# Performance work log

Measured on AMD Instinct MI355X. Metric: run time of the kernel, lower is better.

Reference implementation:

```python
import jax, jax.numpy as jnp
import numpy as np

ITER_NUM = 512
BATCH = 65536
HIDDEN = 256
DELTA_T = 0.1


def setup_inputs() -> dict:
    key = jax.random.key(0)
    k1, k2, k3, k4 = jax.random.split(key, 4)
    inflows = jax.random.uniform(k1, (ITER_NUM, BATCH, 1), dtype=jnp.float32)
    storage0 = jax.random.uniform(k2, (BATCH,), dtype=jnp.float32)
    W1 = jax.random.normal(k3, (2, HIDDEN), dtype=jnp.float32) * 0.5
    b1 = jnp.zeros((HIDDEN,), dtype=jnp.float32)
    W2 = jax.random.normal(k4, (HIDDEN, 1), dtype=jnp.float32) * 0.1
    b2 = jnp.zeros((1,), dtype=jnp.float32)
    return {"inflows": inflows, "storage0": storage0, "W1": W1, "b1": b1, "W2": W2, "b2": b2}


def reference(inflows, storage0, W1, b1, W2, b2):
    # AnnModel: Linear(nx,hidden) -> ReLU -> Linear(hidden,ny)
    def mlp(x):  # x: (B, 2)
        h = jax.nn.relu(x @ W1 + b1)          # (B, H)
        return h @ W2 + b2                     # (B, 1)

    def step(storage, inflow):  # storage: (B,1), inflow: (B,1)
        x = jnp.concatenate([inflow, storage], axis=1)      # (B, 2)
        outflow = mlp(x)                                     # (B, 1)
        storage_new = DELTA_T * (inflow - outflow) + storage # water balance update
        return storage_new, (storage_new, outflow)

    s0 = storage0[:, None]  # (B, 1)
    _, (stor_seq, outflows) = jax.lax.scan(step, s0, inflows)
    storages = jnp.concatenate([s0[None], stor_seq], axis=0)  # (T+1, B, 1)
    return storages, outflows
```

## Files before the change

### kernel.cpp

```cpp
#include <hip/hip_runtime.h>

#define DT 0.1f

typedef float v2f __attribute__((ext_vector_type(2)));

__global__ void pack_weights(const float* __restrict__ W1, const float* __restrict__ b1,
                             const float* __restrict__ W2, float4* __restrict__ ws, int hidden) {
    int j = blockIdx.x * blockDim.x + threadIdx.x;
    if (j < hidden) {
        ws[j] = make_float4(W1[j], W1[hidden + j], b1[j], W2[j]);
    }
}

template <int CTRL>
__device__ __forceinline__ float dpp_add(float x) {
    int v = __builtin_amdgcn_mov_dpp(__float_as_int(x), CTRL, 0xf, 0xf, true);
    return x + __int_as_float(v);
}

__global__ __launch_bounds__(256) void waterbalance(
    const float* __restrict__ inflows, const float* __restrict__ storage0,
    const float4* __restrict__ ws, const float* __restrict__ b2,
    float* __restrict__ out_storages, float* __restrict__ out_outflows,
    int iters, int batch)
{
    const int tid = blockIdx.x * blockDim.x + threadIdx.x;
    const int e = tid >> 3;
    const int p = tid & 7;
    if (e >= batch) return;

    v2f wx[16], wy[16], wb[16], w2[16];
    #pragma unroll
    for (int r = 0; r < 16; ++r) {
        float4 a = ws[p * 32 + 2 * r];
        float4 b = ws[p * 32 + 2 * r + 1];
        wx[r] = (v2f){a.x, b.x};
        wy[r] = (v2f){a.y, b.y};
        wb[r] = (v2f){a.z, b.z};
        w2[r] = (v2f){a.w, b.w};
    }
    const float b2v = b2[0];

    float s = storage0[e];
    if (p == 0) out_storages[e] = s;

    float inflow = inflows[e];
    for (int t = 0; t < iters; ++t) {
        float next = (t + 1 < iters) ? inflows[(size_t)(t + 1) * batch + e] : 0.0f;

        const v2f in2 = (v2f){inflow, inflow};
        const v2f s2  = (v2f){s, s};
        v2f acc0 = (v2f)(0.0f);
        v2f acc1 = (v2f)(0.0f);
        const v2f zero2 = (v2f)(0.0f);

        #pragma unroll
        for (int r = 0; r < 16; r += 2) {
            v2f z0 = __builtin_elementwise_fma(in2, wx[r],
                        __builtin_elementwise_fma(s2, wy[r], wb[r]));
            z0 = __builtin_elementwise_max(z0, zero2);
            acc0 = __builtin_elementwise_fma(z0, w2[r], acc0);

            v2f z1 = __builtin_elementwise_fma(in2, wx[r + 1],
                        __builtin_elementwise_fma(s2, wy[r + 1], wb[r + 1]));
            z1 = __builtin_elementwise_max(z1, zero2);
            acc1 = __builtin_elementwise_fma(z1, w2[r + 1], acc1);
        }

        float part = (acc0.x + acc0.y) + (acc1.x + acc1.y);
        part = dpp_add<0xB1>(part);
        part = dpp_add<0x4E>(part);
        part = dpp_add<0x141>(part);
        const float outflow = part + b2v;

        s = fmaf(DT, inflow - outflow, s);

        if (p == 0) {
            out_outflows[(size_t)t * batch + e] = outflow;
            out_storages[(size_t)(t + 1) * batch + e] = s;
        }
        inflow = next;
    }
}

extern "C" void kernel_launch(void* const* d_in, const int* in_sizes, int n_in,
                              void* d_out, int out_size, void* d_ws, size_t ws_size,
                              hipStream_t stream) {
    const float* inflows  = (const float*)d_in[0];
    const float* storage0 = (const float*)d_in[1];
    const float* W1       = (const float*)d_in[2];
    const float* b1       = (const float*)d_in[3];
    const float* W2       = (const float*)d_in[4];
    const float* b2       = (const float*)d_in[5];

    int batch  = in_sizes[1];
    int iters  = in_sizes[0] / batch;
    int hidden = in_sizes[3];

    float4* ws = (float4*)d_ws;
    pack_weights<<<(hidden + 255) / 256, 256, 0, stream>>>(W1, b1, W2, ws, hidden);

    float* out_storages = (float*)d_out;
    float* out_outflows = out_storages + (size_t)(iters + 1) * batch;

    int threads = batch * 8;
    waterbalance<<<(threads + 255) / 256, 256, 0, stream>>>(
        inflows, storage0, ws, b2, out_storages, out_outflows, iters, batch);
}
```

Before: 1.059 ms.

## Prefetch inflows in chunks of eight and force packed FMA via inline asm

Restructures the time loop into chunks of 8 steps. The next chunk's 8 inflow values are loaded ahead while the current chunk computes, which hides global-load latency behind the serial recurrence better than a one-step prefetch. The MLP FMAs are forced to v_pk_fma_f32 through inline asm, and empty asm barriers pin the weights in VGPRs. The outputs use incremented pointers, which removes index arithmetic. This costs more registers and loses some compiler scheduling freedom around the asm blocks.

```diff
diff --git a/kernel.cpp b/kernel.cpp
--- a/kernel.cpp
+++ b/kernel.cpp
@@ -10,6 +10,12 @@
     if (j < hidden) {
         ws[j] = make_float4(W1[j], W1[hidden + j], b1[j], W2[j]);
     }
+}
+
+__device__ __forceinline__ v2f pk_fma(v2f a, v2f b, v2f c) {
+    v2f d;
+    asm("v_pk_fma_f32 %0, %1, %2, %3" : "=v"(d) : "v"(a), "v"(b), "v"(c));
+    return d;
 }
 
 template <int CTRL>
@@ -39,47 +45,105 @@
         wb[r] = (v2f){a.z, b.z};
         w2[r] = (v2f){a.w, b.w};
     }
+    #pragma unroll
+    for (int r = 0; r < 16; ++r) {
+        asm("" : "+v"(wx[r]), "+v"(wy[r]), "+v"(wb[r]), "+v"(w2[r]));
+    }
+
     const float b2v = b2[0];
 
     float s = storage0[e];
     if (p == 0) out_storages[e] = s;
 
-    float inflow = inflows[e];
-    for (int t = 0; t < iters; ++t) {
-        float next = (t + 1 < iters) ? inflows[(size_t)(t + 1) * batch + e] : 0.0f;
+    const float* __restrict__ inp = inflows + e;
+    float* __restrict__ po = out_outflows + e;
+    float* __restrict__ ps = out_storages + (size_t)batch + e;
 
+    const int nchunk = iters >> 3;
+    const int tail_start = nchunk << 3;
+
+    float buf[8];
+    #pragma unroll
+    for (int r = 0; r < 8; ++r) buf[r] = inp[(size_t)r * batch];
+
+    for (int c = 0; c < nchunk; ++c) {
+        float nb[8];
+        if (c + 1 < nchunk) {
+            const float* q = inp + (size_t)(c + 1) * 8 * batch;
+            #pragma unroll
+            for (int r = 0; r < 8; ++r) nb[r] = q[(size_t)r * batch];
+        } else {
+            #pragma unroll
+            for (int r = 0; r < 8; ++r) nb[r] = 0.0f;
+        }
+
+        #pragma unroll
+        for (int r = 0; r < 8; ++r) {
+            const float inflow = buf[r];
+            const v2f in2 = (v2f){inflow, inflow};
+            const v2f s2  = (v2f){s, s};
+            const v2f zero2 = (v2f)(0.0f);
+            v2f acc0 = (v2f)(0.0f);
+            v2f acc1 = (v2f)(0.0f);
+
+            #pragma unroll
+            for (int g = 0; g < 16; g += 2) {
+                v2f z0 = pk_fma(in2, wx[g], pk_fma(s2, wy[g], wb[g]));
+                z0 = __builtin_elementwise_max(z0, zero2);
+                acc0 = pk_fma(z0, w2[g], acc0);
+
+                v2f z1 = pk_fma(in2, wx[g + 1], pk_fma(s2, wy[g + 1], wb[g + 1]));
+                z1 = __builtin_elementwise_max(z1, zero2);
+                acc1 = pk_fma(z1, w2[g + 1], acc1);
+            }
+
+            float part = (acc0.x + acc1.x) + (acc0.y + acc1.y);
+            part = dpp_add<0xB1>(part);
+            part = dpp_add<0x4E>(part);
+            part = dpp_add<0x141>(part);
+            const float outflow = part + b2v;
+
+            s = fmaf(DT, inflow - outflow, s);
+
+            if (p == 0) {
+                *po = outflow;
+                *ps = s;
+            }
+            po += batch;
+            ps += batch;
+        }
+
+        #pragma unroll
+        for (int r = 0; r < 8; ++r) buf[r] = nb[r];
+    }
+
+    for (int t = tail_start; t < iters; ++t) {
+        const float inflow = inp[(size_t)t * batch];
         const v2f in2 = (v2f){inflow, inflow};
         const v2f s2  = (v2f){s, s};
-        v2f acc0 = (v2f)(0.0f);
-        v2f acc1 = (v2f)(0.0f);
         const v2f zero2 = (v2f)(0.0f);
-
+        v2f acc0 = (v2f)(0.0f), acc1 = (v2f)(0.0f);
         #pragma unroll
-        for (int r = 0; r < 16; r += 2) {
-            v2f z0 = __builtin_elementwise_fma(in2, wx[r],
-                        __builtin_elementwise_fma(s2, wy[r], wb[r]));
+        for (int g = 0; g < 16; g += 2) {
+            v2f z0 = pk_fma(in2, wx[g], pk_fma(s2, wy[g], wb[g]));
             z0 = __builtin_elementwise_max(z0, zero2);
-            acc0 = __builtin_elementwise_fma(z0, w2[r], acc0);
-
-            v2f z1 = __builtin_elementwise_fma(in2, wx[r + 1],
-                        __builtin_elementwise_fma(s2, wy[r + 1], wb[r + 1]));
+            acc0 = pk_fma(z0, w2[g], acc0);
+            v2f z1 = pk_fma(in2, wx[g + 1], pk_fma(s2, wy[g + 1], wb[g + 1]));
             z1 = __builtin_elementwise_max(z1, zero2);
-            acc1 = __builtin_elementwise_fma(z1, w2[r + 1], acc1);
+            acc1 = pk_fma(z1, w2[g + 1], acc1);
         }
-
-        float part = (acc0.x + acc0.y) + (acc1.x + acc1.y);
+        float part = (acc0.x + acc1.x) + (acc0.y + acc1.y);
         part = dpp_add<0xB1>(part);
         part = dpp_add<0x4E>(part);
         part = dpp_add<0x141>(part);
         const float outflow = part + b2v;
-
         s = fmaf(DT, inflow - outflow, s);
-
         if (p == 0) {
-            out_outflows[(size_t)t * batch + e] = outflow;
-            out_storages[(size_t)(t + 1) * batch + e] = s;
+            *po = outflow;
+            *ps = s;
         }
-        inflow = next;
+        po += batch;
+        ps += batch;
     }
 }
 
```

Measured after the change: 1.061 ms. Within noise of the previous version (+0.2%).

## Process four batch elements per 8-lane group to reuse register-resident weights

Applied to the files above, without the earlier changes.

Each group of 8 lanes now handles 4 consecutive batch elements instead of 1, so every weight pair loaded into registers feeds 4 independent FMA chains. This amortizes the per-element loop overhead, gives more instruction-level parallelism, and makes per-thread loads and stores contiguous, at the cost of a 4x smaller grid and higher register pressure. Inline asm emits v_pk_fma_f32 directly, and an empty asm barrier keeps the weights pinned in registers. Batch sizes not divisible by 4 would leave their tail elements unprocessed.

```diff
diff --git a/kernel.cpp b/kernel.cpp
--- a/kernel.cpp
+++ b/kernel.cpp
@@ -12,74 +12,112 @@
     }
 }
 
+__device__ __forceinline__ v2f pk_fma(v2f a, v2f b, v2f c) {
+    v2f d;
+    asm("v_pk_fma_f32 %0, %1, %2, %3" : "=v"(d) : "v"(a), "v"(b), "v"(c));
+    return d;
+}
+
 template <int CTRL>
 __device__ __forceinline__ float dpp_add(float x) {
     int v = __builtin_amdgcn_mov_dpp(__float_as_int(x), CTRL, 0xf, 0xf, true);
     return x + __int_as_float(v);
 }
 
-__global__ __launch_bounds__(256) void waterbalance(
+__global__ __launch_bounds__(256, 2) void waterbalance(
     const float* __restrict__ inflows, const float* __restrict__ storage0,
     const float4* __restrict__ ws, const float* __restrict__ b2,
     float* __restrict__ out_storages, float* __restrict__ out_outflows,
     int iters, int batch)
 {
     const int tid = blockIdx.x * blockDim.x + threadIdx.x;
-    const int e = tid >> 3;
+    const int g = tid >> 3;
     const int p = tid & 7;
-    if (e >= batch) return;
+    const int nquad = batch >> 2;
+    if (g >= nquad) return;
+    const int e0 = g << 2;
 
     v2f wx[16], wy[16], wb[16], w2[16];
     #pragma unroll
-    for (int r = 0; r < 16; ++r) {
-        float4 a = ws[p * 32 + 2 * r];
-        float4 b = ws[p * 32 + 2 * r + 1];
-        wx[r] = (v2f){a.x, b.x};
-        wy[r] = (v2f){a.y, b.y};
-        wb[r] = (v2f){a.z, b.z};
-        w2[r] = (v2f){a.w, b.w};
+    for (int q = 0; q < 16; ++q) {
+        float4 a = ws[p * 32 + 2 * q];
+        float4 b = ws[p * 32 + 2 * q + 1];
+        wx[q] = (v2f){a.x, b.x};
+        wy[q] = (v2f){a.y, b.y};
+        wb[q] = (v2f){a.z, b.z};
+        w2[q] = (v2f){a.w, b.w};
     }
+    #pragma unroll
+    for (int q = 0; q < 16; ++q) {
+        asm("" : "+v"(wx[q]), "+v"(wy[q]), "+v"(wb[q]), "+v"(w2[q]));
+    }
+
     const float b2v = b2[0];
 
-    float s = storage0[e];
-    if (p == 0) out_storages[e] = s;
+    float s[4], cur[4];
+    #pragma unroll
+    for (int r = 0; r < 4; ++r) s[r] = storage0[e0 + r];
+    if (p == 0) {
+        #pragma unroll
+        for (int r = 0; r < 4; ++r) out_storages[e0 + r] = s[r];
+    }
+    #pragma unroll
+    for (int r = 0; r < 4; ++r) cur[r] = inflows[e0 + r];
 
-    float inflow = inflows[e];
     for (int t = 0; t < iters; ++t) {
-        float next = (t + 1 < iters) ? inflows[(size_t)(t + 1) * batch + e] : 0.0f;
+        float nxt[4];
+        if (t + 1 < iters) {
+            const size_t bn = (size_t)(t + 1) * batch + e0;
+            #pragma unroll
+            for (int r = 0; r < 4; ++r) nxt[r] = inflows[bn + r];
+        } else {
+            #pragma unroll
+            for (int r = 0; r < 4; ++r) nxt[r] = 0.0f;
+        }
 
-        const v2f in2 = (v2f){inflow, inflow};
-        const v2f s2  = (v2f){s, s};
-        v2f acc0 = (v2f)(0.0f);
-        v2f acc1 = (v2f)(0.0f);
         const v2f zero2 = (v2f)(0.0f);
+        v2f in2[4], s2[4], acc[4];
+        #pragma unroll
+        for (int r = 0; r < 4; ++r) {
+            in2[r] = (v2f){cur[r], cur[r]};
+            s2[r]  = (v2f){s[r], s[r]};
+            acc[r] = zero2;
+        }
 
         #pragma unroll
-        for (int r = 0; r < 16; r += 2) {
-            v2f z0 = __builtin_elementwise_fma(in2, wx[r],
-                        __builtin_elementwise_fma(s2, wy[r], wb[r]));
-            z0 = __builtin_elementwise_max(z0, zero2);
-            acc0 = __builtin_elementwise_fma(z0, w2[r], acc0);
-
-            v2f z1 = __builtin_elementwise_fma(in2, wx[r + 1],
-                        __builtin_elementwise_fma(s2, wy[r + 1], wb[r + 1]));
-            z1 = __builtin_elementwise_max(z1, zero2);
-            acc1 = __builtin_elementwise_fma(z1, w2[r + 1], acc1);
+        for (int q = 0; q < 16; ++q) {
+            const v2f x = wx[q], y = wy[q], bb = wb[q], w = w2[q];
+            #pragma unroll
+            for (int r = 0; r < 4; ++r) {
+                v2f z = pk_fma(in2[r], x, pk_fma(s2[r], y, bb));
+                z = __builtin_elementwise_max(z, zero2);
+                acc[r] = pk_fma(z, w, acc[r]);
+            }
         }
 
-        float part = (acc0.x + acc0.y) + (acc1.x + acc1.y);
-        part = dpp_add<0xB1>(part);
-        part = dpp_add<0x4E>(part);
-        part = dpp_add<0x141>(part);
-        const float outflow = part + b2v;
-
-        s = fmaf(DT, inflow - outflow, s);
+        float of[4];
+        #pragma unroll
+        for (int r = 0; r < 4; ++r) {
+            float part = acc[r].x + acc[r].y;
+            part = dpp_add<0xB1>(part);
+            part = dpp_add<0x4E>(part);
+            part = dpp_add<0x141>(part);
+            of[r] = part + b2v;
+            s[r] = fmaf(DT, cur[r] - of[r], s[r]);
+        }
 
         if (p == 0) {
-            out_outflows[(size_t)t * batch + e] = outflow;
-            out_storages[(size_t)(t + 1) * batch + e] = s;
+            const size_t ot = (size_t)t * batch + e0;
+            const size_t st = (size_t)(t + 1) * batch + e0;
+            #pragma unroll
+            for (int r = 0; r < 4; ++r) {
+                out_outflows[ot + r] = of[r];
+                out_storages[st + r] = s[r];
+            }
         }
-        inflow = next;
+
+        #pragma unroll
+        for (int r = 0; r < 4; ++r) cur[r] = nxt[r];
     }
 }
 
@@ -103,7 +141,7 @@
     float* out_storages = (float*)d_out;
     float* out_outflows = out_storages + (size_t)(iters + 1) * batch;
 
-    int threads = batch * 8;
+    int threads = (batch / 4) * 8;
     waterbalance<<<(threads + 255) / 256, 256, 0, stream>>>(
         inflows, storage0, ws, b2, out_storages, out_outflows, iters, batch);
 }
```

Measured after the change: 1.149 ms. 8.4% more time.
